# Optimization experiments

Hardware: AMD Instinct MI355X
Metric: run time of the kernel (lower is better)

Reference implementation:

```python
import jax, jax.numpy as jnp
import numpy as np


def setup_inputs() -> dict:
    key = jax.random.key(0)
    k1, k2 = jax.random.split(key)
    B, T, K, D = 8, 4096, 1024, 256
    x = jax.random.normal(k1, (B, T, D), dtype=jnp.float32)
    codebook = jax.random.normal(k2, (K, D), dtype=jnp.float32)
    return {"x": x, "codebook": codebook}


def reference(x, codebook):
    # Faithful to: dist = tf.norm(z_e - lookup_, axis=-1); argmin(dist, -1).
    # argmin of the Euclidean norm == argmin of the squared distance, so we
    # instead of materializing the (B, T, k, d) broadcast intermediate.
    x2 = jnp.sum(x * x, axis=-1, keepdims=True)          # (B, T, 1)
    c2 = jnp.sum(codebook * codebook, axis=-1)           # (k,)
    xc = jnp.einsum('btd,kd->btk', x, codebook)          # (B, T, k)
    dist2 = x2 + c2 - 2.0 * xc                           # (B, T, k)
    return jnp.argmin(dist2, axis=-1)                    # (B, T) int
```

## Files before the change

### kernel.cpp

```cpp
#include <hip/hip_runtime.h>
#include <stdint.h>

typedef __attribute__((ext_vector_type(8))) _Float16 f16x8;
typedef __attribute__((ext_vector_type(4))) float f32x4;

#define MARG 0.09375f

__device__ __forceinline__ void glds16(const void* g, void* l) {
  __builtin_amdgcn_global_load_lds(
      (const __attribute__((address_space(1))) void*)g,
      (__attribute__((address_space(3))) void*)l, 16, 0, 0);
}

__device__ __forceinline__ unsigned short f2h(float f) {
  return __builtin_bit_cast(unsigned short, (_Float16)f);
}

__global__ __launch_bounds__(256) void vq_prep_cb(const float* __restrict__ cb,
                                                  unsigned short* __restrict__ cbh,
                                                  float* __restrict__ hc,
                                                  float* __restrict__ cbT,
                                                  int* __restrict__ count) {
  __shared__ float tile[16][260];
  const int tid = threadIdx.x;
  const int r0 = blockIdx.x * 16;
  const int lane = tid & 63;
  const int wave = tid >> 6;

#pragma unroll
  for (int i = 0; i < 4; ++i) {
    int r = i * 4 + (tid >> 6);
    int d = lane * 4;
    float4 v = *reinterpret_cast<const float4*>(cb + (size_t)(r0 + r) * 256 + d);
    *reinterpret_cast<float4*>(&tile[r][d]) = v;
    ushort4 h;
    h.x = f2h(v.x); h.y = f2h(v.y); h.z = f2h(v.z); h.w = f2h(v.w);
    *reinterpret_cast<ushort4*>(cbh + (size_t)(r0 + r) * 256 + d) = h;
  }
  __syncthreads();

#pragma unroll
  for (int i = 0; i < 4; ++i) {
    int r = wave * 4 + i;
    float4 v = *reinterpret_cast<const float4*>(&tile[r][lane * 4]);
    float s = v.x * v.x + v.y * v.y + v.z * v.z + v.w * v.w;
#pragma unroll
    for (int m = 32; m >= 1; m >>= 1) s += __shfl_xor(s, m, 64);
    if (lane == 0) hc[r0 + r] = 0.5f * s;
  }

  {
    const int d = tid;
#pragma unroll
    for (int i = 0; i < 4; ++i) {
      float4 v = make_float4(tile[i * 4 + 0][d], tile[i * 4 + 1][d],
                             tile[i * 4 + 2][d], tile[i * 4 + 3][d]);
      *reinterpret_cast<float4*>(cbT + (size_t)d * 1024 + r0 + i * 4) = v;
    }
  }
  if (blockIdx.x == 0 && tid == 0) *count = 0;
}

__global__ __launch_bounds__(512, 4) void vq_mfma_kernel(
    const float* __restrict__ x, const unsigned short* __restrict__ cbh,
    const float* __restrict__ hc, int* __restrict__ out,
    int* __restrict__ list, int* __restrict__ count) {
  __shared__ unsigned short Alds[16384];
  __shared__ unsigned short Blds[16384];
  __shared__ float c2s[1024];
  __shared__ float cbv[4][64];
  __shared__ int   cbi[4][64];
  __shared__ float csv[4][64];

  const int tid = threadIdx.x;
  const int lane = tid & 63;
  const int wave = tid >> 6;
  const int wr = wave >> 2;
  const int wc = wave & 3;
  const int l15 = lane & 15;
  const int l4  = lane >> 4;
  const int bswz = (blockIdx.x & 7) * 64 + (blockIdx.x >> 3);
  const int r0 = bswz * 64;

  reinterpret_cast<float2*>(c2s)[tid] = reinterpret_cast<const float2*>(hc)[tid];

  {
    const int row = tid >> 3;
    const int cc  = tid & 7;
    const float* src = x + (size_t)(r0 + row) * 256 + cc * 32;
    unsigned short hv[32];
#pragma unroll
    for (int q = 0; q < 8; ++q) {
      float4 v = *reinterpret_cast<const float4*>(src + q * 4);
      hv[q * 4 + 0] = f2h(v.x); hv[q * 4 + 1] = f2h(v.y);
      hv[q * 4 + 2] = f2h(v.z); hv[q * 4 + 3] = f2h(v.w);
    }
    char* base = reinterpret_cast<char*>(Alds);
#pragma unroll
    for (int g = 0; g < 4; ++g) {
      int byte = (row * 512 + cc * 64 + g * 16) ^ ((row & 7) << 4);
      *reinterpret_cast<f16x8*>(base + byte) = *reinterpret_cast<const f16x8*>(&hv[g * 8]);
    }
  }

  auto stage = [&](int T1) {
    const int p = T1 & 1;
    const int n0 = (T1 >> 3) << 8;
    const int d0 = (T1 & 7) << 5;
    unsigned short* B = Blds + p * 8192;
#pragma unroll
    for (int r = 0; r < 2; ++r) {
      int idx = r * 512 + tid;
      int bch = (idx & 3) ^ ((idx >> 3) & 3);
      glds16(cbh + (size_t)(n0 + (idx >> 2)) * 256 + d0 + bch * 8, B + idx * 8);
    }
  };

  float bestv[2][4], secondv[2][4];
  int besti[2][4];
#pragma unroll
  for (int tr = 0; tr < 2; ++tr)
#pragma unroll
    for (int g = 0; g < 4; ++g) {
      bestv[tr][g] = -3.4e38f; secondv[tr][g] = -3.4e38f; besti[tr][g] = 0;
    }

  __syncthreads();
  stage(0);

  const int swzf = (l15 >> 1) & 3;
  int abase[2];
#pragma unroll
  for (int tr = 0; tr < 2; ++tr) {
    int arow = wr * 32 + tr * 16 + l15;
    abase[tr] = (arow * 512 + l4 * 16) ^ ((arow & 7) << 4);
  }

  int T = 0;
  for (int nt = 0; nt < 4; ++nt) {
    f32x4 acc[2][4];
#pragma unroll
    for (int tr = 0; tr < 2; ++tr)
#pragma unroll
      for (int tc = 0; tc < 4; ++tc) acc[tr][tc] = (f32x4){0.f, 0.f, 0.f, 0.f};

    for (int dt = 0; dt < 8; ++dt, ++T) {
      const int p = T & 1;
      if (T < 31) {
        stage(T + 1);
        asm volatile("s_waitcnt vmcnt(2)" ::: "memory");
      } else {
        asm volatile("s_waitcnt vmcnt(0)" ::: "memory");
      }
      __builtin_amdgcn_s_barrier();

      const char* Ab = reinterpret_cast<const char*>(Alds);
      const unsigned short* B = Blds + p * 8192;

      f16x8 af[2], bf[4];
#pragma unroll
      for (int tr = 0; tr < 2; ++tr)
        af[tr] = *reinterpret_cast<const f16x8*>(Ab + (abase[tr] ^ (dt * 64)));
#pragma unroll
      for (int tc = 0; tc < 4; ++tc) {
        int bcol = wc * 64 + tc * 16 + l15;
        bf[tc] = *reinterpret_cast<const f16x8*>(B + bcol * 32 + (l4 ^ swzf) * 8);
      }

      __builtin_amdgcn_s_setprio(1);
#pragma unroll
      for (int tr = 0; tr < 2; ++tr)
#pragma unroll
        for (int tc = 0; tc < 4; ++tc)
          acc[tr][tc] = __builtin_amdgcn_mfma_f32_16x16x32_f16(af[tr], bf[tc], acc[tr][tc], 0, 0, 0);
      __builtin_amdgcn_s_setprio(0);

      asm volatile("s_waitcnt lgkmcnt(0)" ::: "memory");
      __builtin_amdgcn_s_barrier();
    }

    const int cb0 = nt * 256 + wc * 64 + l15;
    float hcv[4];
#pragma unroll
    for (int tc = 0; tc < 4; ++tc) hcv[tc] = c2s[cb0 + tc * 16];
#pragma unroll
    for (int tr = 0; tr < 2; ++tr)
#pragma unroll
      for (int tc = 0; tc < 4; ++tc) {
        const int code = cb0 + tc * 16;
#pragma unroll
        for (int g = 0; g < 4; ++g) {
          float s = acc[tr][tc][g] - hcv[tc];
          bool gt = s > bestv[tr][g];
          float ns = gt ? bestv[tr][g] : fmaxf(secondv[tr][g], s);
          bestv[tr][g] = gt ? s : bestv[tr][g];
          besti[tr][g] = gt ? code : besti[tr][g];
          secondv[tr][g] = ns;
        }
      }
  }

#pragma unroll
  for (int tr = 0; tr < 2; ++tr)
#pragma unroll
    for (int g = 0; g < 4; ++g) {
      float bv = bestv[tr][g]; int bi = besti[tr][g]; float sv = secondv[tr][g];
#pragma unroll
      for (int m = 1; m < 16; m <<= 1) {
        float ov = __shfl_xor(bv, m, 64);
        int   oi = __shfl_xor(bi, m, 64);
        float os = __shfl_xor(sv, m, 64);
        sv = fmaxf(fmaxf(sv, os), fminf(bv, ov));
        bool gt = (ov > bv) || (ov == bv && oi < bi);
        bv = gt ? ov : bv;
        bi = gt ? oi : bi;
      }
      if (l15 == 0) {
        int rl = wr * 32 + tr * 16 + l4 * 4 + g;
        cbv[wc][rl] = bv; cbi[wc][rl] = bi; csv[wc][rl] = sv;
      }
    }

  __syncthreads();
  if (tid < 64) {
    float bv = cbv[0][tid]; int bi = cbi[0][tid]; float sv = csv[0][tid];
#pragma unroll
    for (int w2 = 1; w2 < 4; ++w2) {
      float ov = cbv[w2][tid]; int oi = cbi[w2][tid]; float os = csv[w2][tid];
      sv = fmaxf(fmaxf(sv, os), fminf(bv, ov));
      bool gt = (ov > bv) || (ov == bv && oi < bi);
      bv = gt ? ov : bv;
      bi = gt ? oi : bi;
    }
    out[r0 + tid] = bi;
    if (sv >= bv - MARG) {
      int slot = atomicAdd(count, 1);
      list[slot] = r0 + tid;
    }
  }
}

__global__ __launch_bounds__(512) void vq_cleanup(const float* __restrict__ x,
                                                  const float* __restrict__ cbT,
                                                  const float* __restrict__ hc,
                                                  const int* __restrict__ list,
                                                  const int* __restrict__ count,
                                                  int* __restrict__ out) {
  __shared__ float xt[4][256];
  __shared__ int rowids[4];
  __shared__ float wbv[8][2];
  __shared__ int   wbi[8][2];
  const int tid = threadIdx.x;
  const int wave = tid >> 6;
  const int half = tid >> 8;
  const int c0 = (tid & 255) * 4;
  const int n = *count;

  for (int t0 = blockIdx.x * 4; t0 < n; t0 += gridDim.x * 4) {
    __syncthreads();
    if (tid < 4) rowids[tid] = (t0 + tid < n) ? list[t0 + tid] : -1;
    __syncthreads();
    {
      int j = tid >> 7, seg = tid & 127;
      int row = rowids[j];
      if (row < 0) row = rowids[0];
      *reinterpret_cast<float2*>(&xt[j][seg * 2]) =
          *reinterpret_cast<const float2*>(x + (size_t)row * 256 + seg * 2);
    }
    __syncthreads();

    float a0[4], a1[4];
#pragma unroll
    for (int k = 0; k < 4; ++k) { a0[k] = 0.f; a1[k] = 0.f; }

    const float4* cvp = reinterpret_cast<const float4*>(cbT) + (c0 >> 2);
    const float* xr0 = &xt[half * 2 + 0][0];
    const float* xr1 = &xt[half * 2 + 1][0];
#pragma unroll 4
    for (int d = 0; d < 256; ++d) {
      float4 cv = cvp[d * 256];
      float x0 = xr0[d];
      float x1 = xr1[d];
      a0[0] = fmaf(cv.x, x0, a0[0]); a0[1] = fmaf(cv.y, x0, a0[1]);
      a0[2] = fmaf(cv.z, x0, a0[2]); a0[3] = fmaf(cv.w, x0, a0[3]);
      a1[0] = fmaf(cv.x, x1, a1[0]); a1[1] = fmaf(cv.y, x1, a1[1]);
      a1[2] = fmaf(cv.z, x1, a1[2]); a1[3] = fmaf(cv.w, x1, a1[3]);
    }

    float4 hcv = *reinterpret_cast<const float4*>(hc + c0);

#pragma unroll
    for (int r = 0; r < 2; ++r) {
      const float* a = (r == 0) ? a0 : a1;
      float bv = a[0] - hcv.x; int bi = c0;
      float s1 = a[1] - hcv.y; if (s1 > bv) { bv = s1; bi = c0 + 1; }
      float s2 = a[2] - hcv.z; if (s2 > bv) { bv = s2; bi = c0 + 2; }
      float s3 = a[3] - hcv.w; if (s3 > bv) { bv = s3; bi = c0 + 3; }
#pragma unroll
      for (int m = 1; m < 64; m <<= 1) {
        float ov = __shfl_xor(bv, m, 64);
        int   oi = __shfl_xor(bi, m, 64);
        bool gt = (ov > bv) || (ov == bv && oi < bi);
        bv = gt ? ov : bv;
        bi = gt ? oi : bi;
      }
      if ((tid & 63) == 0) { wbv[wave][r] = bv; wbi[wave][r] = bi; }
    }
    __syncthreads();
    if (tid < 4 && rowids[tid] >= 0) {
      int h2 = tid >> 1, lr = tid & 1;
      int wbase = h2 * 4;
      float bv = wbv[wbase][lr]; int bi = wbi[wbase][lr];
#pragma unroll
      for (int w2 = 1; w2 < 4; ++w2) {
        float ov = wbv[wbase + w2][lr]; int oi = wbi[wbase + w2][lr];
        if (ov > bv || (ov == bv && oi < bi)) { bv = ov; bi = oi; }
      }
      out[rowids[tid]] = bi;
    }
  }
}

#define BM 128
#define BN 256
#define BD 32
#define NT 512

__global__ __launch_bounds__(256) void vq_c2_kernel(const float* __restrict__ cb,
                                                    float* __restrict__ halfc2) {
  int row  = blockIdx.x * 4 + (threadIdx.x >> 6);
  int lane = threadIdx.x & 63;
  float4 v = *reinterpret_cast<const float4*>(cb + (size_t)row * 256 + lane * 4);
  float s = v.x * v.x + v.y * v.y + v.z * v.z + v.w * v.w;
#pragma unroll
  for (int m = 32; m >= 1; m >>= 1) s += __shfl_xor(s, m, 64);
  if (lane == 0) halfc2[row] = 0.5f * s;
}

__global__ __launch_bounds__(NT, 2) void vq_argmin_kernel(
    const float* __restrict__ x, const float* __restrict__ cb,
    const float* __restrict__ halfc2, int* __restrict__ out) {
  __shared__ float lds[2][(BM + BN) * BD];
  __shared__ float c2s[1024];
  const int tid = threadIdx.x;
  const int w   = tid >> 6;
  const int tc  = tid & 31;
  const int tr  = tid >> 5;
  const int r0  = blockIdx.x * BM;
  reinterpret_cast<float2*>(c2s)[tid] = reinterpret_cast<const float2*>(halfc2)[tid];
  const int sA  = tr & 7;
  const int sB  = tc & 7;
  const int sAB = sA ^ sB;
  const int cho = (((tid & 7) ^ w)) * 4;
  const int sub = tid >> 3;
  float bestv[8]; int besti[8];
#pragma unroll
  for (int i = 0; i < 8; ++i) { bestv[i] = -3.4e38f; besti[i] = 0; }
  auto stage = [&](int n0, int d0, int p) {
    float* dst  = &lds[p][0];
    float* dstB = dst + BM * BD;
#pragma unroll
    for (int r = 0; r < 2; ++r) {
      int t2 = r * NT + tid;
      glds16(x + (size_t)(r0 + r * 64 + sub) * 256 + d0 + cho, dst + t2 * 4);
    }
#pragma unroll
    for (int r = 0; r < 4; ++r) {
      int t2 = r * NT + tid;
      glds16(cb + (size_t)(n0 + r * 64 + sub) * 256 + d0 + cho, dstB + t2 * 4);
    }
  };
  stage(0, 0, 0);
  int t = 0;
  for (int nt = 0; nt < 4; ++nt) {
    float acc[8][8];
#pragma unroll
    for (int i = 0; i < 8; ++i)
#pragma unroll
      for (int j = 0; j < 8; ++j) acc[i][j] = 0.f;
    for (int dt = 0; dt < 8; ++dt, ++t) {
      const int p = t & 1;
      if (t < 31) {
        const int t1 = t + 1;
        stage((t1 >> 3) * BN, (t1 & 7) * BD, t1 & 1);
        asm volatile("s_waitcnt vmcnt(6)" ::: "memory");
      } else {
        asm volatile("s_waitcnt vmcnt(0)" ::: "memory");
      }
      __builtin_amdgcn_s_barrier();
      const float* pA = &lds[p][tr * 8 * BD];
      const float* pB = &lds[p][BM * BD + tc * 8 * BD];
#pragma unroll
      for (int cc = 0; cc < 8; ++cc) {
        const float* pBc = pB + ((cc ^ sAB) << 2);
        float4 a[8], b[8];
#pragma unroll
        for (int i = 0; i < 8; ++i)
          a[i] = *reinterpret_cast<const float4*>(pA + i * BD + cc * 4);
#pragma unroll
        for (int j = 0; j < 8; ++j)
          b[j] = *reinterpret_cast<const float4*>(pBc + j * BD);
#pragma unroll
        for (int i = 0; i < 8; ++i)
#pragma unroll
          for (int j = 0; j < 8; ++j) {
            acc[i][j] = fmaf(a[i].x, b[j].x, acc[i][j]);
            acc[i][j] = fmaf(a[i].y, b[j].y, acc[i][j]);
            acc[i][j] = fmaf(a[i].z, b[j].z, acc[i][j]);
            acc[i][j] = fmaf(a[i].w, b[j].w, acc[i][j]);
          }
      }
      asm volatile("s_waitcnt lgkmcnt(0)" ::: "memory");
      __builtin_amdgcn_s_barrier();
    }
    const int n0 = nt * BN;
#pragma unroll
    for (int j = 0; j < 8; ++j) {
      const int code = n0 + tc * 8 + j;
      const float hc = c2s[code];
#pragma unroll
      for (int i = 0; i < 8; ++i) {
        float s = acc[i][j] - hc;
        if (s > bestv[i]) { bestv[i] = s; besti[i] = code; }
      }
    }
  }
#pragma unroll
  for (int i = 0; i < 8; ++i) {
#pragma unroll
    for (int m = 1; m <= 16; m <<= 1) {
      float ov = __shfl_xor(bestv[i], m, 64);
      int   oi = __shfl_xor(besti[i], m, 64);
      if (ov > bestv[i] || (ov == bestv[i] && oi < besti[i])) { bestv[i] = ov; besti[i] = oi; }
    }
  }
  if (tc == 0) {
#pragma unroll
    for (int i = 0; i < 8; ++i) out[r0 + tr * 8 + i] = besti[i];
  }
}

extern "C" void kernel_launch(void* const* d_in, const int* in_sizes, int n_in,
                              void* d_out, int out_size, void* d_ws, size_t ws_size,
                              hipStream_t stream) {
  const float* x  = (const float*)d_in[0];
  const float* cb = (const float*)d_in[1];
  int* out = (int*)d_out;

  const size_t OFF_CH  = 0;
  const size_t OFF_HC  = OFF_CH + (size_t)1024 * 256 * 2;
  const size_t OFF_CBT = OFF_HC + (size_t)1024 * 4;
  const size_t OFF_LS  = OFF_CBT + (size_t)1024 * 256 * 4;
  const size_t OFF_CT  = OFF_LS + (size_t)32768 * 4;
  const size_t NEED    = OFF_CT + 64;

  if (ws_size >= NEED) {
    unsigned short* cbh = (unsigned short*)((char*)d_ws + OFF_CH);
    float* hc  = (float*)((char*)d_ws + OFF_HC);
    float* cbT = (float*)((char*)d_ws + OFF_CBT);
    int* list  = (int*)((char*)d_ws + OFF_LS);
    int* count = (int*)((char*)d_ws + OFF_CT);

    hipLaunchKernelGGL(vq_prep_cb, dim3(64), dim3(256), 0, stream, cb, cbh, hc, cbT, count);
    hipLaunchKernelGGL(vq_mfma_kernel, dim3(512), dim3(512), 0, stream,
                       x, cbh, hc, out, list, count);
    hipLaunchKernelGGL(vq_cleanup, dim3(1024), dim3(512), 0, stream,
                       x, cbT, hc, list, count, out);
  } else {
    float* c2 = (float*)d_ws;
    hipLaunchKernelGGL(vq_c2_kernel, dim3(256), dim3(256), 0, stream, cb, c2);
    hipLaunchKernelGGL(vq_argmin_kernel, dim3(32768 / BM), dim3(NT), 0, stream,
                       x, cb, c2, out);
  }
}
```

Before: 69.50 us.

## Keep A fragments in registers and deepen codebook pipeline to four LDS stages

Each wave now loads its whole A (x-tile) fragment set into registers once after conversion. This frees the A LDS region, which is reused as two more B staging buffers, so the codebook pipeline goes from double to quad buffering with three tiles prefetched ahead. The change removes per-step A LDS reads and hides more global-load latency. In exchange it costs many more VGPRs, and launch bounds drop from 4 to 2 blocks per CU, which lowers occupancy.

New measurement: 76.01 us. +9.4%, slower.

```diff
diff --git a/kernel.cpp b/kernel.cpp
--- a/kernel.cpp
+++ b/kernel.cpp
@@ -61,12 +61,12 @@
   if (blockIdx.x == 0 && tid == 0) *count = 0;
 }
 
-__global__ __launch_bounds__(512, 4) void vq_mfma_kernel(
+__global__ __launch_bounds__(512, 2) void vq_mfma_kernel(
     const float* __restrict__ x, const unsigned short* __restrict__ cbh,
     const float* __restrict__ hc, int* __restrict__ out,
     int* __restrict__ list, int* __restrict__ count) {
-  __shared__ unsigned short Alds[16384];
-  __shared__ unsigned short Blds[16384];
+  __shared__ unsigned short Blds01[16384];
+  __shared__ unsigned short ABu[16384];
   __shared__ float c2s[1024];
   __shared__ float cbv[4][64];
   __shared__ int   cbi[4][64];
@@ -95,24 +95,37 @@
       hv[q * 4 + 0] = f2h(v.x); hv[q * 4 + 1] = f2h(v.y);
       hv[q * 4 + 2] = f2h(v.z); hv[q * 4 + 3] = f2h(v.w);
     }
-    char* base = reinterpret_cast<char*>(Alds);
+    char* base = reinterpret_cast<char*>(ABu);
 #pragma unroll
     for (int g = 0; g < 4; ++g) {
       int byte = (row * 512 + cc * 64 + g * 16) ^ ((row & 7) << 4);
       *reinterpret_cast<f16x8*>(base + byte) = *reinterpret_cast<const f16x8*>(&hv[g * 8]);
     }
   }
-
-  auto stage = [&](int T1) {
-    const int p = T1 & 1;
+  __syncthreads();
+
+  f16x8 af[2][8];
+  {
+    const char* Ab = reinterpret_cast<const char*>(ABu);
+#pragma unroll
+    for (int tr = 0; tr < 2; ++tr) {
+      int arow = wr * 32 + tr * 16 + l15;
+      int abase = (arow * 512 + l4 * 16) ^ ((arow & 7) << 4);
+#pragma unroll
+      for (int dt = 0; dt < 8; ++dt)
+        af[tr][dt] = *reinterpret_cast<const f16x8*>(Ab + (abase ^ (dt * 64)));
+    }
+  }
+  __syncthreads();
+
+  auto stageTo = [&](int T1, unsigned short* Bd) {
     const int n0 = (T1 >> 3) << 8;
     const int d0 = (T1 & 7) << 5;
-    unsigned short* B = Blds + p * 8192;
 #pragma unroll
     for (int r = 0; r < 2; ++r) {
       int idx = r * 512 + tid;
       int bch = (idx & 3) ^ ((idx >> 3) & 3);
-      glds16(cbh + (size_t)(n0 + (idx >> 2)) * 256 + d0 + bch * 8, B + idx * 8);
+      glds16(cbh + (size_t)(n0 + (idx >> 2)) * 256 + d0 + bch * 8, Bd + idx * 8);
     }
   };
 
@@ -125,18 +138,12 @@
       bestv[tr][g] = -3.4e38f; secondv[tr][g] = -3.4e38f; besti[tr][g] = 0;
     }
 
-  __syncthreads();
-  stage(0);
+  stageTo(0, Blds01);
+  stageTo(1, Blds01 + 8192);
+  stageTo(2, ABu);
 
   const int swzf = (l15 >> 1) & 3;
-  int abase[2];
-#pragma unroll
-  for (int tr = 0; tr < 2; ++tr) {
-    int arow = wr * 32 + tr * 16 + l15;
-    abase[tr] = (arow * 512 + l4 * 16) ^ ((arow & 7) << 4);
-  }
-
-  int T = 0;
+
   for (int nt = 0; nt < 4; ++nt) {
     f32x4 acc[2][4];
 #pragma unroll
@@ -144,23 +151,28 @@
 #pragma unroll
       for (int tc = 0; tc < 4; ++tc) acc[tr][tc] = (f32x4){0.f, 0.f, 0.f, 0.f};
 
-    for (int dt = 0; dt < 8; ++dt, ++T) {
-      const int p = T & 1;
-      if (T < 31) {
-        stage(T + 1);
+#pragma unroll
+    for (int dt = 0; dt < 8; ++dt) {
+      const int T = nt * 8 + dt;
+      const int bS = (dt + 3) & 3;
+      const int bR = dt & 3;
+      if (T <= 28) {
+        unsigned short* Bd = (bS & 2) ? (ABu + (bS & 1) * 8192)
+                                      : (Blds01 + (bS & 1) * 8192);
+        stageTo(T + 3, Bd);
+        asm volatile("s_waitcnt vmcnt(6)" ::: "memory");
+      } else if (dt == 5) {
+        asm volatile("s_waitcnt vmcnt(4)" ::: "memory");
+      } else if (dt == 6) {
         asm volatile("s_waitcnt vmcnt(2)" ::: "memory");
       } else {
         asm volatile("s_waitcnt vmcnt(0)" ::: "memory");
       }
       __builtin_amdgcn_s_barrier();
 
-      const char* Ab = reinterpret_cast<const char*>(Alds);
-      const unsigned short* B = Blds + p * 8192;
-
-      f16x8 af[2], bf[4];
-#pragma unroll
-      for (int tr = 0; tr < 2; ++tr)
-        af[tr] = *reinterpret_cast<const f16x8*>(Ab + (abase[tr] ^ (dt * 64)));
+      const unsigned short* B = (bR & 2) ? (ABu + (bR & 1) * 8192)
+                                         : (Blds01 + (bR & 1) * 8192);
+      f16x8 bf[4];
 #pragma unroll
       for (int tc = 0; tc < 4; ++tc) {
         int bcol = wc * 64 + tc * 16 + l15;
@@ -172,7 +184,8 @@
       for (int tr = 0; tr < 2; ++tr)
 #pragma unroll
         for (int tc = 0; tc < 4; ++tc)
-          acc[tr][tc] = __builtin_amdgcn_mfma_f32_16x16x32_f16(af[tr], bf[tc], acc[tr][tc], 0, 0, 0);
+          acc[tr][tc] = __builtin_amdgcn_mfma_f32_16x16x32_f16(
+              af[tr][dt], bf[tc], acc[tr][tc], 0, 0, 0);
       __builtin_amdgcn_s_setprio(0);
 
       asm volatile("s_waitcnt lgkmcnt(0)" ::: "memory");
```
